# Optimization experiments

Hardware: AMD Instinct MI355X
Metric: run time of the kernel (lower is better)

Reference implementation:

```python
import jax, jax.numpy as jnp
import numpy as np

N_QUBITS = 6
N_LAYERS = 4
N_ACTIONS = 4
PRE_DIM = 64
BATCH = 262144


def _cnot(state, ctrl, tgt):
    # state: (B, 2,...,2); flip target axis on the control=1 slice
    ca, ta = 1 + ctrl, 1 + tgt
    s0 = jnp.take(state, 0, axis=ca)
    s1 = jnp.take(state, 1, axis=ca)
    ta_in = ta if ta < ca else ta - 1
    s1 = jnp.flip(s1, axis=ta_in)
    return jnp.stack([s0, s1], axis=ca)


def _ry_batched(state, angles_q, q):
    # angles_q: (B,) per-sample RY angle on qubit q (AngleEmbedding)
    h = angles_q * 0.5
    c, s = jnp.cos(h), jnp.sin(h)
    R = jnp.stack([jnp.stack([c, -s], -1), jnp.stack([s, c], -1)], -2)  # (B,2,2)
    st = jnp.moveaxis(state, 1 + q, -1)
    st = jnp.einsum('b...i,bji->b...j', st, R)
    return jnp.moveaxis(st, -1, 1 + q)


def _ry_scalar(state, theta, q):
    h = theta * 0.5
    c, s = jnp.cos(h), jnp.sin(h)
    R = jnp.stack([jnp.stack([c, -s]), jnp.stack([s, c])])  # (2,2)
    st = jnp.moveaxis(state, 1 + q, -1)
    st = st @ R.T  # new_j = sum_i R[j,i] amp_i
    return jnp.moveaxis(st, -1, 1 + q)


def _circuit(xp, qw):
    # xp: (B, n_qubits) angles; qw: (n_layers, n_qubits)
    B = xp.shape[0]
    state = jnp.zeros((B,) + (2,) * N_QUBITS, xp.dtype)
    state = state.at[(slice(None),) + (0,) * N_QUBITS].set(1.0)
    for q in range(N_QUBITS):
        state = _ry_batched(state, xp[:, q], q)
    for l in range(N_LAYERS):
        for i in range(N_QUBITS):
            state = _cnot(state, i, (i + 1) % N_QUBITS)
        for i in range(N_QUBITS):
            state = _ry_scalar(state, qw[l, i], i)
    probs = state * state  # RY/CNOT are real; state stays real
    all_axes = tuple(range(1, N_QUBITS + 1))
    zs = []
    for q in range(N_QUBITS):
        p = jnp.sum(probs, axis=tuple(a for a in all_axes if a != 1 + q))  # (B,2)
        zs.append(p[:, 0] - p[:, 1])
    return jnp.stack(zs, -1)  # (B, n_qubits)


def setup_inputs() -> dict:
    key = jax.random.key(0)
    ks = jax.random.split(key, 10)
    x = jax.random.normal(ks[0], (BATCH, N_QUBITS), jnp.float32)
    sc = 1.0 / np.sqrt(N_QUBITS)
    W1 = jax.random.uniform(ks[1], (PRE_DIM, N_QUBITS), jnp.float32, -sc, sc)
    b1 = jax.random.uniform(ks[2], (PRE_DIM,), jnp.float32, -sc, sc)
    sc2 = 1.0 / np.sqrt(PRE_DIM)
    W2 = jax.random.uniform(ks[3], (N_QUBITS, PRE_DIM), jnp.float32, -sc2, sc2)
    b2 = jax.random.uniform(ks[4], (N_QUBITS,), jnp.float32, -sc2, sc2)
    qw = jax.random.uniform(ks[5], (N_LAYERS, N_QUBITS), jnp.float32, 0.0, 2.0 * np.pi)
    Wp = jax.random.uniform(ks[6], (N_ACTIONS, N_QUBITS), jnp.float32, -sc, sc)
    bp = jax.random.uniform(ks[7], (N_ACTIONS,), jnp.float32, -sc, sc)
    Wv = jax.random.uniform(ks[8], (1, N_QUBITS), jnp.float32, -sc, sc)
    bv = jax.random.uniform(ks[9], (1,), jnp.float32, -sc, sc)
    return {"x": x, "W1": W1, "b1": b1, "W2": W2, "b2": b2, "qw": qw,
            "Wp": Wp, "bp": bp, "Wv": Wv, "bv": bv}


def reference(x, W1, b1, W2, b2, qw, Wp, bp, Wv, bv):
    h = jax.nn.relu(x @ W1.T + b1)
    xp = jax.nn.relu(h @ W2.T + b2)          # (B, n_qubits)
    qout = _circuit(xp, qw)                   # (B, n_qubits)
    policy = jax.nn.softmax(qout @ Wp.T + bp, axis=-1)
    value = (qout @ Wv.T + bv)[:, 0]
    return policy, value
```

## Files before the change

kernel.cpp:

```cpp
#include <hip/hip_runtime.h>
#include <math.h>


#define NQ 6
#define NL 4
#define NA 4
#define PD 64

typedef float v2 __attribute__((ext_vector_type(2)));

__device__ __forceinline__ v2 mk2(float a, float b) { v2 r; r.x = a; r.y = b; return r; }
__device__ __forceinline__ v2 pkfma(v2 a, v2 b, v2 c) { return __builtin_elementwise_fma(a, b, c); }

__device__ __forceinline__ float dppx1(float v) {
    int i = __builtin_bit_cast(int, v);
    i = __builtin_amdgcn_mov_dpp(i, 0xB1, 0xF, 0xF, true);
    return __builtin_bit_cast(float, i);
}

__global__ __launch_bounds__(256) void mlp_kernel(
    const float* __restrict__ x,
    const float* __restrict__ W1,
    const float* __restrict__ b1,
    const float* __restrict__ W2,
    const float* __restrict__ b2,
    const float* __restrict__ qw,
    float* __restrict__ ws,
    int B)
{
    const int s = blockIdx.x * blockDim.x + threadIdx.x;

    if (blockIdx.x == 0 && threadIdx.x < NL * NQ) {
        const int l = threadIdx.x / NQ, i = threadIdx.x % NQ;
        const float hh0 = 0.5f * qw[l * NQ + i];
        float* dst = ws + l * 16;
        if (i == 0) {
            dst[0] = cosf(hh0);
            dst[1] = sinf(hh0);
        } else {
            const float hh = (hh0 > 1.5707963f) ? (hh0 - 3.14159265358979f) : hh0;
            const float sh = sinf(hh), ch = cosf(hh);
            dst[2 * i]     = -sh / (1.0f + ch);
            dst[2 * i + 1] = sh;
        }
    }
    if (s >= B) return;

    const v2* xv = reinterpret_cast<const v2*>(x + (size_t)s * NQ);
    const v2 x01 = xv[0], x23 = xv[1], x45 = xv[2];

    const v2* W1v = reinterpret_cast<const v2*>(W1);
    const v2* W2v = reinterpret_cast<const v2*>(W2);

    v2 xpa[NQ];
#pragma unroll
    for (int i = 0; i < NQ; ++i) xpa[i] = mk2(b2[i], 0.0f);
#pragma unroll
    for (int k2 = 0; k2 < PD / 2; ++k2) {
        float hu[2];
#pragma unroll
        for (int u = 0; u < 2; ++u) {
            const int j = 2 * k2 + u;
            v2 acc = mk2(b1[j], 0.0f);
            acc = pkfma(x01, W1v[j * 3 + 0], acc);
            acc = pkfma(x23, W1v[j * 3 + 1], acc);
            acc = pkfma(x45, W1v[j * 3 + 2], acc);
            hu[u] = fmaxf(acc.x + acc.y, 0.0f);
        }
        const v2 hv = mk2(hu[0], hu[1]);
#pragma unroll
        for (int i = 0; i < NQ; ++i)
            xpa[i] = pkfma(hv, W2v[i * (PD / 2) + k2], xpa[i]);
    }

    v2* xpo = reinterpret_cast<v2*>(ws + 256) + (size_t)s * 3;
#pragma unroll
    for (int i = 0; i < 3; ++i)
        xpo[i] = mk2(fmaxf(xpa[2 * i].x     + xpa[2 * i].y,     0.0f),
                     fmaxf(xpa[2 * i + 1].x + xpa[2 * i + 1].y, 0.0f));
}

__global__ __launch_bounds__(256) void qpolicy_kernel(
    const float* __restrict__ ws,
    const float* __restrict__ Wp,
    const float* __restrict__ bp,
    const float* __restrict__ Wv,
    const float* __restrict__ bv,
    float* __restrict__ out,
    int B)
{
    const int t = blockIdx.x * blockDim.x + threadIdx.x;
    const int s = t >> 1;
    const bool podd = (t & 1) != 0;

    const v2* xpv = reinterpret_cast<const v2*>(ws + 256) + (size_t)s * 3;
    const v2 p01 = xpv[0], p23 = xpv[1], p45 = xpv[2];
    const float xp[NQ] = { p01.x, p01.y, p23.x, p23.y, p45.x, p45.y };

    float cq[NQ], sq[NQ];
#pragma unroll
    for (int q = 0; q < NQ; ++q) __sincosf(0.5f * xp[q], &sq[q], &cq[q]);

    {
        const float c1 = podd ? sq[1] : cq[1];
        const float s1 = podd ? cq[1] : sq[1];
        cq[1] = c1; sq[1] = s1;
    }

    const float g0 = podd ? sq[0] : cq[0];
    float pr[16];
    pr[0] = g0;
#pragma unroll
    for (int q = 1; q <= 4; ++q) {
        const int sz = 1 << (q - 1);
#pragma unroll
        for (int k = sz - 1; k >= 0; --k) {
            const float v = pr[k];
            pr[2 * k]     = v * cq[q];
            pr[2 * k + 1] = v * sq[q];
        }
    }
    v2 st[16];
    const v2 cs5 = mk2(cq[5], sq[5]);
#pragma unroll
    for (int j = 0; j < 16; ++j) st[j] = mk2(pr[j], pr[j]) * cs5;

#pragma unroll
    for (int l = 0; l < NL; ++l) {
        const float* cst = ws + l * 16;

        if (l > 0) {
#pragma unroll
            for (int j = 0; j < 8; ++j) {
                const v2 a = st[j], b = st[j | 8];
                st[j]     = podd ? b : a;
                st[j | 8] = podd ? a : b;
            }
        }
#pragma unroll
        for (int j = 0; j < 16; ++j)
            if ((j & 8) && !(j & 4)) { v2 tmp = st[j]; st[j] = st[j | 4]; st[j | 4] = tmp; }
#pragma unroll
        for (int j = 0; j < 16; ++j)
            if ((j & 4) && !(j & 2)) { v2 tmp = st[j]; st[j] = st[j | 2]; st[j | 2] = tmp; }
#pragma unroll
        for (int j = 0; j < 16; ++j)
            if ((j & 2) && !(j & 1)) { v2 tmp = st[j]; st[j] = st[j | 2 - 1]; st[j | 1] = tmp; }
#pragma unroll
        for (int j = 0; j < 16; ++j)
            if (j & 1) st[j] = __builtin_shufflevector(st[j], st[j], 1, 0);

        {
            const float c0r = cst[0], s0r = cst[1];
            const float ssg = podd ? s0r : -s0r;
            const v2 c2 = mk2(c0r, c0r), sg2 = mk2(ssg, ssg);
#pragma unroll
            for (int j = 0; j < 16; ++j) {
                const float px = dppx1(st[j].x);
                const float py = dppx1(st[j].y);
                const v2 A  = mk2(st[j].x, py);
                const v2 Bv = mk2(px, st[j].y);
                st[j] = pkfma(sg2, Bv, A * c2);
            }
        }
#pragma unroll
        for (int i = 1; i <= 4; ++i) {
            const int m = 1 << (4 - i);
            const v2 vnt = mk2(cst[2 * i], cst[2 * i]);
            const v2 vs  = mk2(cst[2 * i + 1], cst[2 * i + 1]);
#pragma unroll
            for (int j = 0; j < 16; ++j) {
                if (!(j & m)) {
                    v2 a = st[j], b = st[j | m];
                    a = pkfma(vnt, b, a);
                    b = pkfma(vs, a, b);
                    a = pkfma(vnt, b, a);
                    st[j] = a; st[j | m] = b;
                }
            }
        }
        {
            const float nt = cst[10], s5 = cst[11];
#pragma unroll
            for (int j = 0; j < 16; ++j) {
                float a0 = st[j].x, a1 = st[j].y;
                a0 = fmaf(nt, a1, a0);
                a1 = fmaf(s5, a0, a1);
                a0 = fmaf(nt, a1, a0);
                st[j] = mk2(a0, a1);
            }
        }
    }

    float a[16];
    float S5l = 0.0f;
#pragma unroll
    for (int j = 0; j < 16; ++j) {
        const v2 pp = st[j] * st[j];
        a[j] = pp.x + pp.y;
        S5l += pp.x;
    }
    float S1l = 0.0f;
#pragma unroll
    for (int j = 0; j < 8; ++j) S1l += a[j];
    float b8[8];
#pragma unroll
    for (int j = 0; j < 8; ++j) b8[j] = a[j] + a[j | 8];
    const float S2l = b8[0] + b8[1] + b8[2] + b8[3];
    float b4[4];
#pragma unroll
    for (int j = 0; j < 4; ++j) b4[j] = b8[j] + b8[j | 4];
    const float S3l = b4[0] + b4[1];
    float b2v[2];
    b2v[0] = b4[0] + b4[2];
    b2v[1] = b4[1] + b4[3];
    const float S4l = b2v[0];
    const float Tl  = b2v[0] + b2v[1];

    const float To = dppx1(Tl);
    const float T  = Tl + To;
    const float S0 = podd ? To : Tl;
    const float S1 = S1l + dppx1(S1l);
    const float S2 = S2l + dppx1(S2l);
    const float S3 = S3l + dppx1(S3l);
    const float S4 = S4l + dppx1(S4l);
    const float S5 = S5l + dppx1(S5l);

    float z[NQ];
    z[0] = fmaf(2.0f, S0, -T);
    z[1] = fmaf(2.0f, S1, -T);
    z[2] = fmaf(2.0f, S2, -T);
    z[3] = fmaf(2.0f, S3, -T);
    z[4] = fmaf(2.0f, S4, -T);
    z[5] = fmaf(2.0f, S5, -T);

    float logits[NA];
#pragma unroll
    for (int aidx = 0; aidx < NA; ++aidx) {
        float acc = bp[aidx];
#pragma unroll
        for (int q = 0; q < NQ; ++q) acc = fmaf(z[q], Wp[aidx * NQ + q], acc);
        logits[aidx] = acc;
    }
    float m = logits[0];
#pragma unroll
    for (int aidx = 1; aidx < NA; ++aidx) m = fmaxf(m, logits[aidx]);
    float e[NA];
    float esum = 0.0f;
#pragma unroll
    for (int aidx = 0; aidx < NA; ++aidx) { e[aidx] = __expf(logits[aidx] - m); esum += e[aidx]; }
    const float inv = 1.0f / esum;

    float4 pol;
    pol.x = e[0] * inv; pol.y = e[1] * inv; pol.z = e[2] * inv; pol.w = e[3] * inv;

    float v = bv[0];
#pragma unroll
    for (int q = 0; q < NQ; ++q) v = fmaf(z[q], Wv[q], v);

    if (!podd) {
        reinterpret_cast<float4*>(out)[s] = pol;
        out[(size_t)B * NA + s] = v;
    }
}

extern "C" void kernel_launch(void* const* d_in, const int* in_sizes, int n_in,
                              void* d_out, int out_size, void* d_ws, size_t ws_size,
                              hipStream_t stream) {
    const float* x  = (const float*)d_in[0];
    const float* W1 = (const float*)d_in[1];
    const float* b1 = (const float*)d_in[2];
    const float* W2 = (const float*)d_in[3];
    const float* b2 = (const float*)d_in[4];
    const float* qw = (const float*)d_in[5];
    const float* Wp = (const float*)d_in[6];
    const float* bp = (const float*)d_in[7];
    const float* Wv = (const float*)d_in[8];
    const float* bv = (const float*)d_in[9];
    float* out = (float*)d_out;
    float* ws  = (float*)d_ws;

    const int B = in_sizes[0] / NQ;

    hipLaunchKernelGGL(mlp_kernel, dim3((B + 255) / 256), dim3(256), 0, stream,
                       x, W1, b1, W2, b2, qw, ws, B);

    hipLaunchKernelGGL(qpolicy_kernel, dim3((2 * B + 255) / 256), dim3(256), 0, stream,
                       ws, Wp, bp, Wv, bv, out, B);
}
```

Baseline: 101.8 us.

## Precompute angle sin/cos in MLP kernel and pack circuit math into v2 ops

The MLP kernel now computes the half-angle sincos of each embedding angle and writes cos/sin pairs to the workspace. The circuit kernel then builds the product state directly from those pairs with packed multiplies, so the two threads sharing a sample no longer both evaluate the trig. The qubit-5 rotation changes from a three-FMA shear form to a packed cos/sin rotation, with matching constants written in the setup branch. The probability reductions and the qubit-0 DPP mixing are also packed into two-wide vector ops. In exchange, the intermediate buffer doubles in size, adding global write and read traffic between the two kernels.

```diff
diff --git a/kernel.cpp b/kernel.cpp
--- a/kernel.cpp
+++ b/kernel.cpp
@@ -9,10 +9,10 @@
 
 typedef float v2 __attribute__((ext_vector_type(2)));
 
-__device__ __forceinline__ v2 mk2(float a, float b) { v2 r; r.x = a; r.y = b; return r; }
-__device__ __forceinline__ v2 pkfma(v2 a, v2 b, v2 c) { return __builtin_elementwise_fma(a, b, c); }
-
-__device__ __forceinline__ float dppx1(float v) {
+static __device__ __forceinline__ v2 mk2(float a, float b) { v2 r; r.x = a; r.y = b; return r; }
+static __device__ __forceinline__ v2 pkfma(v2 a, v2 b, v2 c) { return __builtin_elementwise_fma(a, b, c); }
+
+static __device__ __forceinline__ float dppx1(float v) {
     int i = __builtin_bit_cast(int, v);
     i = __builtin_amdgcn_mov_dpp(i, 0xB1, 0xF, 0xF, true);
     return __builtin_bit_cast(float, i);
@@ -37,6 +37,9 @@
         if (i == 0) {
             dst[0] = cosf(hh0);
             dst[1] = sinf(hh0);
+        } else if (i == 5) {
+            dst[10] = cosf(hh0);
+            dst[11] = sinf(hh0);
         } else {
             const float hh = (hh0 > 1.5707963f) ? (hh0 - 3.14159265358979f) : hh0;
             const float sh = sinf(hh), ch = cosf(hh);
@@ -73,11 +76,18 @@
             xpa[i] = pkfma(hv, W2v[i * (PD / 2) + k2], xpa[i]);
     }
 
-    v2* xpo = reinterpret_cast<v2*>(ws + 256) + (size_t)s * 3;
+    float cs[12];
+#pragma unroll
+    for (int i = 0; i < NQ; ++i) {
+        const float xp = fmaxf(xpa[i].x + xpa[i].y, 0.0f);
+        float sh, ch;
+        __sincosf(0.5f * xp, &sh, &ch);
+        cs[2 * i] = ch; cs[2 * i + 1] = sh;
+    }
+    float4* o = reinterpret_cast<float4*>(ws + 256) + (size_t)s * 3;
 #pragma unroll
     for (int i = 0; i < 3; ++i)
-        xpo[i] = mk2(fmaxf(xpa[2 * i].x     + xpa[2 * i].y,     0.0f),
-                     fmaxf(xpa[2 * i + 1].x + xpa[2 * i + 1].y, 0.0f));
+        o[i] = make_float4(cs[4 * i], cs[4 * i + 1], cs[4 * i + 2], cs[4 * i + 3]);
 }
 
 __global__ __launch_bounds__(256) void qpolicy_kernel(
@@ -93,37 +103,32 @@
     const int s = t >> 1;
     const bool podd = (t & 1) != 0;
 
-    const v2* xpv = reinterpret_cast<const v2*>(ws + 256) + (size_t)s * 3;
-    const v2 p01 = xpv[0], p23 = xpv[1], p45 = xpv[2];
-    const float xp[NQ] = { p01.x, p01.y, p23.x, p23.y, p45.x, p45.y };
-
-    float cq[NQ], sq[NQ];
-#pragma unroll
-    for (int q = 0; q < NQ; ++q) __sincosf(0.5f * xp[q], &sq[q], &cq[q]);
-
-    {
-        const float c1 = podd ? sq[1] : cq[1];
-        const float s1 = podd ? cq[1] : sq[1];
-        cq[1] = c1; sq[1] = s1;
-    }
-
-    const float g0 = podd ? sq[0] : cq[0];
-    float pr[16];
-    pr[0] = g0;
-#pragma unroll
-    for (int q = 1; q <= 4; ++q) {
-        const int sz = 1 << (q - 1);
-#pragma unroll
-        for (int k = sz - 1; k >= 0; --k) {
-            const float v = pr[k];
-            pr[2 * k]     = v * cq[q];
-            pr[2 * k + 1] = v * sq[q];
-        }
-    }
-    v2 st[16];
-    const v2 cs5 = mk2(cq[5], sq[5]);
-#pragma unroll
-    for (int j = 0; j < 16; ++j) st[j] = mk2(pr[j], pr[j]) * cs5;
+    const v2* csv = reinterpret_cast<const v2*>(ws + 256) + (size_t)s * 6;
+    v2 cs[6];
+#pragma unroll
+    for (int q = 0; q < 6; ++q) cs[q] = csv[q];
+
+    const float g0 = podd ? cs[0].y : cs[0].x;
+    const v2 cs1f = podd ? __builtin_shufflevector(cs[1], cs[1], 1, 0) : cs[1];
+    const v2 e1 = mk2(g0, g0) * cs1f;
+    v2 e2[2], e3[4], e4[8], st[16];
+    e2[0] = mk2(e1.x, e1.x) * cs[2];
+    e2[1] = mk2(e1.y, e1.y) * cs[2];
+#pragma unroll
+    for (int k = 0; k < 2; ++k) {
+        e3[2 * k]     = mk2(e2[k].x, e2[k].x) * cs[3];
+        e3[2 * k + 1] = mk2(e2[k].y, e2[k].y) * cs[3];
+    }
+#pragma unroll
+    for (int k = 0; k < 4; ++k) {
+        e4[2 * k]     = mk2(e3[k].x, e3[k].x) * cs[4];
+        e4[2 * k + 1] = mk2(e3[k].y, e3[k].y) * cs[4];
+    }
+#pragma unroll
+    for (int k = 0; k < 8; ++k) {
+        st[2 * k]     = mk2(e4[k].x, e4[k].x) * cs[5];
+        st[2 * k + 1] = mk2(e4[k].y, e4[k].y) * cs[5];
+    }
 
 #pragma unroll
     for (int l = 0; l < NL; ++l) {
@@ -139,30 +144,30 @@
         }
 #pragma unroll
         for (int j = 0; j < 16; ++j)
-            if ((j & 8) && !(j & 4)) { v2 tmp = st[j]; st[j] = st[j | 4]; st[j | 4] = tmp; }
-#pragma unroll
-        for (int j = 0; j < 16; ++j)
-            if ((j & 4) && !(j & 2)) { v2 tmp = st[j]; st[j] = st[j | 2]; st[j | 2] = tmp; }
-#pragma unroll
-        for (int j = 0; j < 16; ++j)
-            if ((j & 2) && !(j & 1)) { v2 tmp = st[j]; st[j] = st[j | 2 - 1]; st[j | 1] = tmp; }
+            if ((j & 8) && !(j & 4)) { v2 tm = st[j]; st[j] = st[j | 4]; st[j | 4] = tm; }
+#pragma unroll
+        for (int j = 0; j < 16; ++j)
+            if ((j & 4) && !(j & 2)) { v2 tm = st[j]; st[j] = st[j | 2]; st[j | 2] = tm; }
+#pragma unroll
+        for (int j = 0; j < 16; ++j)
+            if ((j & 2) && !(j & 1)) { v2 tm = st[j]; st[j] = st[j | 1]; st[j | 1] = tm; }
 #pragma unroll
         for (int j = 0; j < 16; ++j)
             if (j & 1) st[j] = __builtin_shufflevector(st[j], st[j], 1, 0);
 
         {
-            const float c0r = cst[0], s0r = cst[1];
-            const float ssg = podd ? s0r : -s0r;
-            const v2 c2 = mk2(c0r, c0r), sg2 = mk2(ssg, ssg);
+            const float c0 = cst[0], s0 = cst[1];
+            const float ssg = podd ? s0 : -s0;
+            const v2 KA = mk2(c0, ssg);
+            const v2 KB = mk2(ssg, c0);
 #pragma unroll
             for (int j = 0; j < 16; ++j) {
-                const float px = dppx1(st[j].x);
-                const float py = dppx1(st[j].y);
-                const v2 A  = mk2(st[j].x, py);
-                const v2 Bv = mk2(px, st[j].y);
-                st[j] = pkfma(sg2, Bv, A * c2);
-            }
-        }
+                const float dx = dppx1(st[j].x);
+                const float dy = dppx1(st[j].y);
+                st[j] = pkfma(KB, mk2(dx, dy), KA * st[j]);
+            }
+        }
+
 #pragma unroll
         for (int i = 1; i <= 4; ++i) {
             const int m = 1 << (4 - i);
@@ -180,42 +185,44 @@
             }
         }
         {
-            const float nt = cst[10], s5 = cst[11];
+            const float c5 = cst[10], s5 = cst[11];
+            const v2 ms  = mk2(-s5, s5);
+            const v2 vc5 = mk2(c5, c5);
 #pragma unroll
             for (int j = 0; j < 16; ++j) {
-                float a0 = st[j].x, a1 = st[j].y;
-                a0 = fmaf(nt, a1, a0);
-                a1 = fmaf(s5, a0, a1);
-                a0 = fmaf(nt, a1, a0);
-                st[j] = mk2(a0, a1);
-            }
-        }
-    }
-
-    float a[16];
-    float S5l = 0.0f;
-#pragma unroll
-    for (int j = 0; j < 16; ++j) {
-        const v2 pp = st[j] * st[j];
-        a[j] = pp.x + pp.y;
-        S5l += pp.x;
-    }
-    float S1l = 0.0f;
-#pragma unroll
-    for (int j = 0; j < 8; ++j) S1l += a[j];
-    float b8[8];
-#pragma unroll
-    for (int j = 0; j < 8; ++j) b8[j] = a[j] + a[j | 8];
-    const float S2l = b8[0] + b8[1] + b8[2] + b8[3];
-    float b4[4];
-#pragma unroll
-    for (int j = 0; j < 4; ++j) b4[j] = b8[j] + b8[j | 4];
-    const float S3l = b4[0] + b4[1];
-    float b2v[2];
-    b2v[0] = b4[0] + b4[2];
-    b2v[1] = b4[1] + b4[3];
-    const float S4l = b2v[0];
-    const float Tl  = b2v[0] + b2v[1];
+                const v2 sw = __builtin_shufflevector(st[j], st[j], 1, 0);
+                st[j] = pkfma(ms, sw, st[j] * vc5);
+            }
+        }
+    }
+
+    v2 asq[16];
+#pragma unroll
+    for (int j = 0; j < 16; ++j) asq[j] = st[j] * st[j];
+
+    v2 s1a = asq[0];
+#pragma unroll
+    for (int j = 1; j < 8; ++j) s1a += asq[j];
+    v2 c8[8];
+#pragma unroll
+    for (int j = 0; j < 8; ++j) c8[j] = asq[j] + asq[j | 8];
+    v2 c4[4];
+#pragma unroll
+    for (int j = 0; j < 4; ++j) c4[j] = c8[j] + c8[j | 4];
+    const v2 s2a = (c8[0] + c8[1]) + (c8[2] + c8[3]);
+    v2 c2[2];
+    c2[0] = c4[0] + c4[2];
+    c2[1] = c4[1] + c4[3];
+    const v2 s3a = c4[0] + c4[1];
+    const v2 s4a = c2[0];
+    const v2 ta  = c2[0] + c2[1];
+
+    const float Tl  = ta.x + ta.y;
+    const float S5l = ta.x;
+    const float S1l = s1a.x + s1a.y;
+    const float S2l = s2a.x + s2a.y;
+    const float S3l = s3a.x + s3a.y;
+    const float S4l = s4a.x + s4a.y;
 
     const float To = dppx1(Tl);
     const float T  = Tl + To;
```

New measurement: 106.0 us. 1.04x slower.
